# Optimization experiments

Hardware: AMD Instinct MI355X
Metric: run time of the kernel (lower is better)

## Reference

```python
import jax, jax.numpy as jnp
import numpy as np

B, T, C = 2, 2048, 1024
H, DH = 16, 64          # n_heads = d_model // 64
WIN = 256               # sliding window size
K = 32                  # n_oscillators
DFF = 4096              # d_ff_hidden
NEG = -1e9


def setup_inputs() -> dict:
    key = jax.random.key(0)
    ks = jax.random.split(key, 16)
    sC = 1.0 / np.sqrt(C)
    sF = 1.0 / np.sqrt(DFF)
    sK = 1.0 / np.sqrt(K)
    return {
        "x": jax.random.normal(ks[0], (B, T, C), jnp.float32),
        "norm1_w": jnp.ones((C,), jnp.float32),
        "qkv_w": jax.random.normal(ks[1], (3 * C, C), jnp.float32) * sC,
        "qkv_b": jnp.zeros((3 * C,), jnp.float32),
        "proj_w": jax.random.normal(ks[2], (C, C), jnp.float32) * sC,
        "proj_b": jnp.zeros((C,), jnp.float32),
        "gate_w": jax.random.normal(ks[3], (1, C), jnp.float32) * 0.01,
        "gate_b": jnp.zeros((1,), jnp.float32),
        "trn_win": jax.random.normal(ks[4], (K, C), jnp.float32) * sC,
        "trn_wout": jax.random.normal(ks[5], (C, K), jnp.float32) * sK,
        "trn_gate_w": jax.random.normal(ks[6], (K, C), jnp.float32) * sC,
        "trn_gate_b": jnp.zeros((K,), jnp.float32),
        "trn_a_logit": jax.random.normal(ks[7], (K,), jnp.float32),
        "trn_theta": jax.random.uniform(ks[8], (K,), jnp.float32, 0.0, np.pi),
        "trn_res_scale": jnp.asarray(0.1, jnp.float32),
        "norm2_w": jnp.ones((C,), jnp.float32),
        "ffn_gate_w": jax.random.normal(ks[9], (DFF, C), jnp.float32) * sC,
        "ffn_up_w": jax.random.normal(ks[10], (DFF, C), jnp.float32) * sC,
        "ffn_down_w": jax.random.normal(ks[11], (C, DFF), jnp.float32) * sF,
    }


def _rms(z, w, eps=1e-6):
    return z * jax.lax.rsqrt(jnp.mean(z * z, axis=-1, keepdims=True) + eps) * w


def reference(x, norm1_w, qkv_w, qkv_b, proj_w, proj_b, gate_w, gate_b,
              trn_win, trn_wout, trn_gate_w, trn_gate_b, trn_a_logit,
              trn_theta, trn_res_scale, norm2_w, ffn_gate_w, ffn_up_w,
              ffn_down_w):
    h = _rms(x, norm1_w)

    # ---- windowed causal attention (dense mask, as in the original) ----
    qkv = h @ qkv_w.T + qkv_b                       # [B,T,3C]
    q, k, v = jnp.split(qkv, 3, axis=-1)
    heads = lambda t: t.reshape(B, T, H, DH).transpose(0, 2, 1, 3)  # [B,H,T,DH]
    q, k, v = heads(q), heads(k), heads(v)
    row = jnp.arange(T)[:, None]
    col = jnp.arange(T)[None, :]
    mask = jnp.where((col <= row) & (col >= row - WIN + 1), 0.0, NEG).astype(x.dtype)
    scores = jnp.einsum('bhqd,bhkd->bhqk', q, k) / jnp.sqrt(jnp.asarray(DH, x.dtype))
    attn = jax.nn.softmax(scores + mask, axis=-1)
    ao = jnp.einsum('bhqk,bhkd->bhqd', attn, v).transpose(0, 2, 1, 3).reshape(B, T, C)
    ao = ao @ proj_w.T + proj_b

    # ---- temporal resonance branch: K damped rotating oscillators ----
    u = h @ trn_win.T                               # [B,T,K] drive
    a = jax.nn.sigmoid(trn_a_logit)                 # amplitude in (0,1) (amplitude_max=1)
    ct, st = jnp.cos(trn_theta), jnp.sin(trn_theta)

    def step(carry, ut):
        sr, si = carry
        nsr = a * (ct * sr - st * si) + ut
        nsi = a * (st * sr + ct * si)
        return (nsr, nsi), nsr

    init = (jnp.zeros((B, K), x.dtype), jnp.zeros((B, K), x.dtype))
    _, ys = jax.lax.scan(step, init, u.transpose(1, 0, 2))  # ys: [T,B,K]
    y = ys.transpose(1, 0, 2)                                # [B,T,K]
    tg = jax.nn.sigmoid(h @ trn_gate_w.T + trn_gate_b)
    trn_out = ((tg * y) @ trn_wout.T) * trn_res_scale        # [B,T,C]

    # ---- sigmoid gate mix + residual ----
    g = jax.nn.sigmoid(h @ gate_w.T + gate_b)       # [B,T,1]
    x = x + g * ao + (1.0 - g) * trn_out

    # ---- SwiGLU FFN ----
    h2 = _rms(x, norm2_w)
    ffn = (jax.nn.silu(h2 @ ffn_gate_w.T) * (h2 @ ffn_up_w.T)) @ ffn_down_w.T
    return x + ffn
```

## Files before the change

### kernel.cpp

```cpp
#include <hip/hip_runtime.h>


typedef unsigned short u16;
typedef unsigned short u16x8 __attribute__((ext_vector_type(8)));
typedef __bf16 bf16x8 __attribute__((ext_vector_type(8)));
typedef float f32x4 __attribute__((ext_vector_type(4)));

#define DI static __device__ __forceinline__

DI u16 f2b(float f){
  union { float f; unsigned u; } v; v.f = f;
  unsigned r = v.u + 0x7FFFu + ((v.u >> 16) & 1u);
  return (u16)(r >> 16);
}
DI float b2f(u16 b){
  union { unsigned u; float f; } v; v.u = ((unsigned)b) << 16; return v.f;
}
DI u16x8 ld8(const u16* p){ return *(const u16x8*)p; }

DI f32x4 MFMA16(u16x8 a, u16x8 b, f32x4 c){
  return __builtin_amdgcn_mfma_f32_16x16x32_bf16(
      __builtin_bit_cast(bf16x8, a), __builtin_bit_cast(bf16x8, b), c, 0, 0, 0);
}

DI void async16(const void* g, void* l){
  void* gg = const_cast<void*>(g);
  __builtin_amdgcn_global_load_lds(
      (__attribute__((address_space(1))) void*)gg,
      (__attribute__((address_space(3))) void*)l, 16, 0, 0);
}

__global__ __launch_bounds__(256) void convert_w(
    const float* __restrict__ qkvw, const float* __restrict__ projw,
    const float* __restrict__ fgw, const float* __restrict__ fuw,
    const float* __restrict__ fdw, const float* __restrict__ twin,
    const float* __restrict__ tgw, const float* __restrict__ twout,
    u16* __restrict__ dst)
{
  size_t i = (size_t)blockIdx.x * 256 + threadIdx.x;
  if (i >= 4260352u) return;
  size_t e = i * 4;
  float4 v;
  if (e < 3145728u)        v = *(const float4*)(qkvw + e);
  else if (e < 4194304u)   v = *(const float4*)(projw + (e - 3145728u));
  else if (e < 12582912u){
    size_t i2 = e - 4194304u;
    int row = (int)(i2 >> 10), c = (int)(i2 & 1023);
    int G = row >> 5, j = row & 31;
    const float* src = (j < 16) ? fgw : fuw;
    v = *(const float4*)(src + (size_t)(G * 16 + (j & 15)) * 1024 + c);
  }
  else if (e < 16777216u)  v = *(const float4*)(fdw + (e - 12582912u));
  else if (e < 16908288u){
    size_t i2 = e - 16777216u;
    int row = (int)(i2 >> 10), c = (int)(i2 & 1023);
    if (row < 32)      v = *(const float4*)(twin + row * 1024 + c);
    else if (row < 64) v = *(const float4*)(tgw + (row - 32) * 1024 + c);
    else               v = make_float4(0.f, 0.f, 0.f, 0.f);
  } else {
    v = *(const float4*)(twout + (e - 16908288u));
  }
  uint2 p;
  p.x = (unsigned)f2b(v.x) | ((unsigned)f2b(v.y) << 16);
  p.y = (unsigned)f2b(v.z) | ((unsigned)f2b(v.w) << 16);
  *(uint2*)(dst + e) = p;
}

__global__ __launch_bounds__(256) void zero_f32(float* __restrict__ p, int n4)
{
  int i = blockIdx.x * 256 + threadIdx.x;
  if (i < n4) ((float4*)p)[i] = make_float4(0.f, 0.f, 0.f, 0.f);
}

__global__ __launch_bounds__(256) void rmsnorm_gate(
    const float* __restrict__ x, const float* __restrict__ w,
    const float* __restrict__ gw, const float* __restrict__ gb,
    u16* __restrict__ h, float* __restrict__ g)
{
  const int row = blockIdx.x, tid = threadIdx.x;
  const int wave = tid >> 6, lane = tid & 63;
  __shared__ float sb[8];
  float4 xv = ((const float4*)(x + (size_t)row * 1024))[tid];
  float ss = xv.x*xv.x + xv.y*xv.y + xv.z*xv.z + xv.w*xv.w;
#pragma unroll
  for (int m = 32; m; m >>= 1) ss += __shfl_xor(ss, m);
  if (lane == 0) sb[wave] = ss;
  __syncthreads();
  float rstd = rsqrtf((sb[0]+sb[1]+sb[2]+sb[3]) * (1.f/1024.f) + 1e-6f);
  float4 wv = ((const float4*)w)[tid];
  float h0 = xv.x*rstd*wv.x, h1 = xv.y*rstd*wv.y;
  float h2v = xv.z*rstd*wv.z, h3 = xv.w*rstd*wv.w;
  uint2 pk;
  pk.x = (unsigned)f2b(h0) | ((unsigned)f2b(h1) << 16);
  pk.y = (unsigned)f2b(h2v) | ((unsigned)f2b(h3) << 16);
  ((uint2*)(h + (size_t)row * 1024))[tid] = pk;
  float4 gv = ((const float4*)gw)[tid];
  float gd = h0*gv.x + h1*gv.y + h2v*gv.z + h3*gv.w;
#pragma unroll
  for (int m = 32; m; m >>= 1) gd += __shfl_xor(gd, m);
  if (lane == 0) sb[4 + wave] = gd;
  __syncthreads();
  if (tid == 0) g[row] = 1.f / (1.f + __expf(-(sb[4]+sb[5]+sb[6]+sb[7] + gb[0])));
}

__global__ __launch_bounds__(256) void reduce_mix_norm(
    const float* __restrict__ part, const float* __restrict__ x,
    const u16* __restrict__ trn, const float* __restrict__ g,
    const float* __restrict__ pb, const float* __restrict__ n2w,
    float* __restrict__ xmid, u16* __restrict__ h2)
{
  const int row = blockIdx.x, tid = threadIdx.x;
  const int wave = tid >> 6, lane = tid & 63;
  __shared__ float sb[4];
  const size_t ro = (size_t)row * 1024;
  float4 p0 = ((const float4*)(part + ro))[tid];
  float4 p1 = ((const float4*)(part + 4194304 + ro))[tid];
  float4 bb = ((const float4*)pb)[tid];
  float4 xv = ((const float4*)(x + ro))[tid];
  uint2 tz = ((const uint2*)(trn + ro))[tid];
  float gg = g[row];
  float t0 = b2f((u16)tz.x), t1 = b2f((u16)(tz.x >> 16));
  float t2 = b2f((u16)tz.y), t3 = b2f((u16)(tz.y >> 16));
  float m0 = xv.x + gg*(p0.x+p1.x+bb.x) + (1.f-gg)*t0;
  float m1 = xv.y + gg*(p0.y+p1.y+bb.y) + (1.f-gg)*t1;
  float m2 = xv.z + gg*(p0.z+p1.z+bb.z) + (1.f-gg)*t2;
  float m3 = xv.w + gg*(p0.w+p1.w+bb.w) + (1.f-gg)*t3;
  float4 mo; mo.x = m0; mo.y = m1; mo.z = m2; mo.w = m3;
  ((float4*)(xmid + ro))[tid] = mo;
  float ss = m0*m0 + m1*m1 + m2*m2 + m3*m3;
#pragma unroll
  for (int m = 32; m; m >>= 1) ss += __shfl_xor(ss, m);
  if (lane == 0) sb[wave] = ss;
  __syncthreads();
  float rstd = rsqrtf((sb[0]+sb[1]+sb[2]+sb[3]) * (1.f/1024.f) + 1e-6f);
  float4 wv = ((const float4*)n2w)[tid];
  uint2 pk;
  pk.x = (unsigned)f2b(m0*rstd*wv.x) | ((unsigned)f2b(m1*rstd*wv.y) << 16);
  pk.y = (unsigned)f2b(m2*rstd*wv.z) | ((unsigned)f2b(m3*rstd*wv.w) << 16);
  ((uint2*)(h2 + ro))[tid] = pk;
}

__global__ __launch_bounds__(256) void reduce_down(
    const float* __restrict__ part, const float* __restrict__ xmid,
    float* __restrict__ out)
{
  size_t i = (size_t)blockIdx.x * 256 + threadIdx.x;
  float4 p0 = ((const float4*)part)[i];
  float4 p1 = ((const float4*)(part + 4194304))[i];
  float4 xv = ((const float4*)xmid)[i];
  float4 o;
  o.x = xv.x + p0.x + p1.x; o.y = xv.y + p0.y + p1.y;
  o.z = xv.z + p0.z + p1.z; o.w = xv.w + p0.w + p1.w;
  ((float4*)out)[i] = o;
}

template<int MODE>
__global__ __launch_bounds__(256) void gemm_bt(
    const u16* __restrict__ A, const u16* __restrict__ B,
    float* __restrict__ outF, float* __restrict__ outF2, u16* __restrict__ outB,
    const float* __restrict__ bias, const float* __restrict__ auxF,
    int M, int N, int K)
{
  __shared__ __align__(16) u16 sA[128 * 32];
  __shared__ __align__(16) u16 sB[128 * 32];
  const int tid = threadIdx.x;
  const int wave = tid >> 6, lane = tid & 63;
  const int lr = lane & 15, lq = lane >> 4;
  const int m0 = blockIdx.x * 128, n0 = blockIdx.y * 128;
  const int wm = (wave & 1) * 64, wn = (wave >> 1) * 64;
  const int ks = K / (int)gridDim.z;
  const int kbeg = (int)blockIdx.z * ks, kend = kbeg + ks;
  f32x4 acc[4][4] = {};
  const int srow = wave * 16 + (lane >> 2);
  const int scol = (lane & 3) * 8;
  const u16* gA = A + (size_t)(m0 + srow) * K + scol;
  const u16* gB = B + (size_t)(n0 + srow) * K + scol;
  u16* lA0 = &sA[(wave * 16) * 32];
  u16* lA1 = &sA[(64 + wave * 16) * 32];
  u16* lB0 = &sB[(wave * 16) * 32];
  u16* lB1 = &sB[(64 + wave * 16) * 32];
  const size_t K64 = (size_t)64 * K;

  for (int k0 = kbeg; k0 < kend; k0 += 32){
    async16(gA + k0,       lA0);
    async16(gA + K64 + k0, lA1);
    async16(gB + k0,       lB0);
    async16(gB + K64 + k0, lB1);
    __syncthreads();
    u16x8 af[4], bf[4];
#pragma unroll
    for (int i = 0; i < 4; i++) af[i] = ld8(&sA[(wm + i*16 + lr)*32 + lq*8]);
#pragma unroll
    for (int i = 0; i < 4; i++) bf[i] = ld8(&sB[(wn + i*16 + lr)*32 + lq*8]);
#pragma unroll
    for (int mi = 0; mi < 4; mi++)
#pragma unroll
      for (int ni = 0; ni < 4; ni++)
        acc[mi][ni] = MFMA16(af[mi], bf[ni], acc[mi][ni]);
    __syncthreads();
  }

  if (MODE == 7){
    const int cb = ((n0 + wn) >> 1) + lr;
#pragma unroll
    for (int mi = 0; mi < 4; mi++){
      const int row = m0 + wm + mi*16 + lq*4;
#pragma unroll
      for (int p = 0; p < 2; p++){
        const int col = cb + p*16;
#pragma unroll
        for (int r = 0; r < 4; r++){
          float gv = acc[mi][2*p][r], uv = acc[mi][2*p+1][r];
          float rv = gv / (1.f + __expf(-gv)) * uv;
          outB[(size_t)(row + r) * (N >> 1) + col] = f2b(rv);
        }
      }
    }
    return;
  }

  float scale6 = 0.f;
  if (MODE == 6) scale6 = auxF[0];

#pragma unroll
  for (int mi = 0; mi < 4; mi++){
    const int row = m0 + wm + mi*16 + lq*4;
#pragma unroll
    for (int ni = 0; ni < 4; ni++){
      const int col = n0 + wn + ni*16 + lr;
#pragma unroll
      for (int r = 0; r < 4; r++){
        const int rr = row + r;
        float v = acc[mi][ni][r];
        if (MODE == 0){
          outB[(size_t)rr * N + col] = f2b(v + bias[col]);
        } else if (MODE == 5){
          int bb = rr >> 11, tt = rr & 2047;
          if (col < 32) atomicAdd(&outF[((size_t)bb * 32 + col) * 2048 + tt], v);
          else if (col < 64) atomicAdd(&outF2[(size_t)rr * 32 + (col - 32)], v);
        } else if (MODE == 6){
          outB[(size_t)rr * N + col] = f2b(v * scale6);
        } else if (MODE == 8){
          outF[(size_t)blockIdx.z * (size_t)M + (size_t)rr * N + col] = v;
        }
      }
    }
  }
}

__global__ __launch_bounds__(256) void attn_win(
    const u16* __restrict__ qkv, u16* __restrict__ ao)
{
  const int blk = blockIdx.x;
  const int tile = blk & 31, hh = (blk >> 5) & 15, b = blk >> 9;
  const int t0 = tile * 64;
  const int tid = threadIdx.x, wave = tid >> 6, lane = tid & 63;
  const int lr = lane & 15, lq = lane >> 4;
  const int qt = t0 + wave * 16;
  __shared__ __align__(16) u16 sVt[64 * 40];
  __shared__ __align__(16) u16 sP[4][16 * 32];

  const u16* base = qkv + (size_t)b * 2048 * 3072 + hh * 64;
  const u16* qrow = base + (size_t)(qt + lr) * 3072 + lq * 8;
  u16x8 qf0 = ld8(qrow), qf1 = ld8(qrow + 32);
  const u16* kbase = base + 1024;
  const u16* vbase = base + 2048;

  f32x4 o0 = {0,0,0,0}, o1 = {0,0,0,0}, o2 = {0,0,0,0}, o3 = {0,0,0,0};
  float mrun[4] = {-1e30f, -1e30f, -1e30f, -1e30f};
  float lrun[4] = {0.f, 0.f, 0.f, 0.f};
  const float c1 = 0.125f * 1.44269504088896f;

  const int kb = (t0 >= 256) ? (t0 - 256) : 0;
  const int ntl = (t0 + 64 - kb) >> 5;
  for (int it = 0; it < ntl; ++it){
    const int kt = kb + it * 32;
    __syncthreads();
    if (tid < 128){
      const int key = tid & 31, dh = tid >> 5;
      const u16* gv = vbase + (size_t)(kt + key) * 3072 + dh * 16;
      u16x8 v0 = ld8(gv), v1 = ld8(gv + 8);
#pragma unroll
      for (int j = 0; j < 8; j++){
        sVt[(dh*16 + j)     * 40 + key] = v0[j];
        sVt[(dh*16 + 8 + j) * 40 + key] = v1[j];
      }
    }
    __syncthreads();
    const bool active = (kt < qt + 16) && (kt + 286 >= qt);
    if (!active) continue;

    f32x4 s0 = {0,0,0,0}, s1 = {0,0,0,0};
    {
      const u16* kr = kbase + (size_t)(kt + lr) * 3072 + lq * 8;
      u16x8 k00 = ld8(kr), k01 = ld8(kr + 32);
      const u16* kr1 = kr + (size_t)16 * 3072;
      u16x8 k10 = ld8(kr1), k11 = ld8(kr1 + 32);
      s0 = MFMA16(qf0, k00, s0); s0 = MFMA16(qf1, k01, s0);
      s1 = MFMA16(qf0, k10, s1); s1 = MFMA16(qf1, k11, s1);
    }
    float al[4];
#pragma unroll
    for (int r = 0; r < 4; r++){
      const int q = qt + lq * 4 + r;
      const int ca = kt + lr, cb = kt + 16 + lr;
      float a0 = (ca <= q && ca + 255 >= q) ? s0[r] : -1e30f;
      float a1 = (cb <= q && cb + 255 >= q) ? s1[r] : -1e30f;
      float mx = fmaxf(a0, a1);
      mx = fmaxf(mx, __shfl_xor(mx, 1));
      mx = fmaxf(mx, __shfl_xor(mx, 2));
      mx = fmaxf(mx, __shfl_xor(mx, 4));
      mx = fmaxf(mx, __shfl_xor(mx, 8));
      float mn = fmaxf(mrun[r], mx);
      al[r] = exp2f((mrun[r] - mn) * c1);
      mrun[r] = mn;
      float p0 = (a0 > -1e29f) ? exp2f((a0 - mn) * c1) : 0.f;
      float p1 = (a1 > -1e29f) ? exp2f((a1 - mn) * c1) : 0.f;
      float sm = p0 + p1;
      sm += __shfl_xor(sm, 1); sm += __shfl_xor(sm, 2);
      sm += __shfl_xor(sm, 4); sm += __shfl_xor(sm, 8);
      lrun[r] = lrun[r] * al[r] + sm;
      sP[wave][(lq*4 + r) * 32 + lr]      = f2b(p0);
      sP[wave][(lq*4 + r) * 32 + 16 + lr] = f2b(p1);
    }
#pragma unroll
    for (int r = 0; r < 4; r++){
      o0[r] *= al[r]; o1[r] *= al[r]; o2[r] *= al[r]; o3[r] *= al[r];
    }
    __builtin_amdgcn_s_waitcnt(0xc07f);
    u16x8 pf = ld8(&sP[wave][lr * 32 + lq * 8]);
    o0 = MFMA16(pf, ld8(&sVt[(lr)      * 40 + lq * 8]), o0);
    o1 = MFMA16(pf, ld8(&sVt[(16 + lr) * 40 + lq * 8]), o1);
    o2 = MFMA16(pf, ld8(&sVt[(32 + lr) * 40 + lq * 8]), o2);
    o3 = MFMA16(pf, ld8(&sVt[(48 + lr) * 40 + lq * 8]), o3);
  }

  u16* aor = ao + (size_t)(b * 2048 + qt + lq * 4) * 1024 + hh * 64 + lr;
#pragma unroll
  for (int r = 0; r < 4; r++){
    float inv = 1.f / lrun[r];
    u16* p = aor + (size_t)r * 1024;
    p[0]  = f2b(o0[r] * inv);
    p[16] = f2b(o1[r] * inv);
    p[32] = f2b(o2[r] * inv);
    p[48] = f2b(o3[r] * inv);
  }
}

__global__ __launch_bounds__(256) void scan_k(
    const float* __restrict__ u_t, const float* __restrict__ tgl,
    const float* __restrict__ tgb,
    const float* __restrict__ alog, const float* __restrict__ theta,
    u16* __restrict__ z)
{
  const int bk = blockIdx.x;
  const int b = bk >> 5, k = bk & 31;
  const int j = threadIdx.x;
  const float a = 1.f / (1.f + __expf(-alog[k]));
  const float th = theta[k];
  const float bk_bias = tgb[k];
  const float wr = a * __cosf(th), wi = a * __sinf(th);
  const float* ubp = u_t + ((size_t)b * 32 + k) * 2048 + j * 8;
  float4 ua = ((const float4*)ubp)[0];
  float4 ub4 = ((const float4*)ubp)[1];
  float ur[8] = {ua.x, ua.y, ua.z, ua.w, ub4.x, ub4.y, ub4.z, ub4.w};
  float sr = 0.f, si = 0.f;
#pragma unroll
  for (int i = 0; i < 8; i++){
    float nr = wr*sr - wi*si + ur[i];
    float ni = wi*sr + wr*si;
    sr = nr; si = ni;
  }
  float w2r = wr*wr - wi*wi, w2i = 2.f*wr*wi;
  float w4r = w2r*w2r - w2i*w2i, w4i = 2.f*w2r*w2i;
  float Ar = w4r*w4r - w4i*w4i, Ai = 2.f*w4r*w4i;
  __shared__ float4 sc[256];
  float4 cur; cur.x = Ar; cur.y = Ai; cur.z = sr; cur.w = si;
  sc[j] = cur;
  __syncthreads();
  for (int s = 1; s < 256; s <<= 1){
    float4 pv;
    const bool has = (j >= s);
    if (has) pv = sc[j - s];
    __syncthreads();
    if (has){
      float nar = cur.x*pv.x - cur.y*pv.y;
      float nai = cur.x*pv.y + cur.y*pv.x;
      float nbr = cur.x*pv.z - cur.y*pv.w + cur.z;
      float nbi = cur.x*pv.w + cur.y*pv.z + cur.w;
      cur.x = nar; cur.y = nai; cur.z = nbr; cur.w = nbi;
    }
    sc[j] = cur;
    __syncthreads();
  }
  float s_r = 0.f, s_i = 0.f;
  if (j > 0){ float4 pr = sc[j - 1]; s_r = pr.z; s_i = pr.w; }
  const float* tgp = tgl + ((size_t)b * 2048 + j * 8) * 32 + k;
  u16* zp = z + ((size_t)b * 2048 + j * 8) * 32 + k;
#pragma unroll
  for (int i = 0; i < 8; i++){
    float nr = wr*s_r - wi*s_i + ur[i];
    float ni = wi*s_r + wr*s_i;
    s_r = nr; s_i = ni;
    float tgv = 1.f / (1.f + __expf(-(tgp[(size_t)i * 32] + bk_bias)));
    zp[(size_t)i * 32] = f2b(s_r * tgv);
  }
}

extern "C" void kernel_launch(void* const* d_in, const int* in_sizes, int n_in,
                              void* d_out, int out_size, void* d_ws, size_t ws_size,
                              hipStream_t stream)
{
  (void)in_sizes; (void)n_in; (void)out_size; (void)ws_size;
  const float* x      = (const float*)d_in[0];
  const float* n1w    = (const float*)d_in[1];
  const float* qkvw   = (const float*)d_in[2];
  const float* qkvb   = (const float*)d_in[3];
  const float* projw  = (const float*)d_in[4];
  const float* projb  = (const float*)d_in[5];
  const float* gatew  = (const float*)d_in[6];
  const float* gateb  = (const float*)d_in[7];
  const float* twin   = (const float*)d_in[8];
  const float* twout  = (const float*)d_in[9];
  const float* tgw    = (const float*)d_in[10];
  const float* tgb    = (const float*)d_in[11];
  const float* talog  = (const float*)d_in[12];
  const float* ttheta = (const float*)d_in[13];
  const float* tscale = (const float*)d_in[14];
  const float* n2w    = (const float*)d_in[15];
  const float* fgw    = (const float*)d_in[16];
  const float* fuw    = (const float*)d_in[17];
  const float* fdw    = (const float*)d_in[18];
  float* out = (float*)d_out;

  char* wsb = (char*)d_ws;
  size_t off = 0;
  auto take = [&](size_t bytes) -> void* {
    void* r = wsb + off; off += (bytes + 255) & ~(size_t)255; return r;
  };
  u16*   wall = (u16*)take(17041408ull * 2);
  u16*   h    = (u16*)take(4194304ull * 2);
  u16*   h2   = (u16*)take(4194304ull * 2);
  u16*   trn  = (u16*)take(4194304ull * 2);
  float* g    = (float*)take(4096ull * 4);
  float* xmid = (float*)take(4194304ull * 4);
  float* uacc = (float*)take(262144ull * 4);
  float* tgl  = uacc + 131072;
  u16*   zz   = (u16*)take(131072ull * 2);
  u16*   regA = (u16*)take(4096ull * 4096 * 2);
  u16*   regB = (u16*)take(4096ull * 4096 * 2);

  u16* wq  = wall;
  u16* wp  = wall + 3145728;
  u16* wgu = wall + 4194304;
  u16* wd  = wall + 12582912;
  u16* wct = wall + 16777216;
  u16* wo  = wall + 16908288;
  u16*   qkv   = regA;
  float* pproj = (float*)regA;
  u16*   act   = regA;
  u16*   ao    = regB;
  float* pdown = (float*)regB;

  convert_w<<<16642, 256, 0, stream>>>(qkvw, projw, fgw, fuw, fdw, twin, tgw, twout, wall);
  rmsnorm_gate<<<4096, 256, 0, stream>>>(x, n1w, gatew, gateb, h, g);
  zero_f32<<<256, 256, 0, stream>>>(uacc, 65536);
  gemm_bt<5><<<dim3(32, 1, 8), 256, 0, stream>>>(h, wct, uacc, tgl, nullptr, nullptr,
                                                 nullptr, 0, 128, 1024);
  scan_k<<<64, 256, 0, stream>>>(uacc, tgl, tgb, talog, ttheta, zz);
  gemm_bt<6><<<dim3(32, 8), 256, 0, stream>>>(zz, wo, nullptr, nullptr, trn, nullptr,
                                              tscale, 0, 1024, 32);
  gemm_bt<0><<<dim3(32, 24), 256, 0, stream>>>(h, wq, nullptr, nullptr, qkv, qkvb,
                                               nullptr, 0, 3072, 1024);
  attn_win<<<1024, 256, 0, stream>>>(qkv, ao);
  gemm_bt<8><<<dim3(32, 8, 2), 256, 0, stream>>>(ao, wp, pproj, nullptr, nullptr, nullptr,
                                                 nullptr, 4194304, 1024, 1024);
  reduce_mix_norm<<<4096, 256, 0, stream>>>(pproj, x, trn, g, projb, n2w, xmid, h2);
  gemm_bt<7><<<dim3(32, 64), 256, 0, stream>>>(h2, wgu, nullptr, nullptr, act, nullptr,
                                               nullptr, 0, 8192, 1024);
  gemm_bt<8><<<dim3(32, 8, 2), 256, 0, stream>>>(act, wd, pdown, nullptr, nullptr, nullptr,
                                                 nullptr, 4194304, 1024, 4096);
  reduce_down<<<4096, 256, 0, stream>>>(pdown, xmid, out);
}
```

Before: 449.6 us.

## Fuse TRN projections into QKV GEMM, widen K-step, atomically accumulate FFN down

Folds the oscillator drive and gate projections into extra columns of the QKV GEMM, so the separate zero-fill and atomic projection GEMM disappear, and moves the gate sigmoid into that epilogue. GEMMs gain a WIDE mode that loads two 32-wide K slabs per barrier pair, halving synchronisation. The FFN down projection now atomically adds into the output, which already holds the residual, with a 4-way K split, removing the reduce_down kernel and the xmid buffer. The attention V-transpose load is also spread across all 256 threads. The atomics make the results order-nondeterministic and add contention.

```diff
diff --git a/kernel.cpp b/kernel.cpp
--- a/kernel.cpp
+++ b/kernel.cpp
@@ -38,38 +38,31 @@
     u16* __restrict__ dst)
 {
   size_t i = (size_t)blockIdx.x * 256 + threadIdx.x;
-  if (i >= 4260352u) return;
+  if (i >= 4235264u) return;
   size_t e = i * 4;
   float4 v;
   if (e < 3145728u)        v = *(const float4*)(qkvw + e);
-  else if (e < 4194304u)   v = *(const float4*)(projw + (e - 3145728u));
-  else if (e < 12582912u){
-    size_t i2 = e - 4194304u;
+  else if (e < 3276800u){
+    size_t i2 = e - 3145728u;
+    int row = (int)(i2 >> 10), c = (int)(i2 & 1023);
+    if (row < 32)      v = *(const float4*)(twin + row * 1024 + c);
+    else if (row < 64) v = *(const float4*)(tgw + (row - 32) * 1024 + c);
+    else               v = make_float4(0.f, 0.f, 0.f, 0.f);
+  }
+  else if (e < 4325376u)   v = *(const float4*)(projw + (e - 3276800u));
+  else if (e < 12713984u){
+    size_t i2 = e - 4325376u;
     int row = (int)(i2 >> 10), c = (int)(i2 & 1023);
     int G = row >> 5, j = row & 31;
     const float* src = (j < 16) ? fgw : fuw;
     v = *(const float4*)(src + (size_t)(G * 16 + (j & 15)) * 1024 + c);
   }
-  else if (e < 16777216u)  v = *(const float4*)(fdw + (e - 12582912u));
-  else if (e < 16908288u){
-    size_t i2 = e - 16777216u;
-    int row = (int)(i2 >> 10), c = (int)(i2 & 1023);
-    if (row < 32)      v = *(const float4*)(twin + row * 1024 + c);
-    else if (row < 64) v = *(const float4*)(tgw + (row - 32) * 1024 + c);
-    else               v = make_float4(0.f, 0.f, 0.f, 0.f);
-  } else {
-    v = *(const float4*)(twout + (e - 16908288u));
-  }
+  else if (e < 16908288u)  v = *(const float4*)(fdw + (e - 12713984u));
+  else                     v = *(const float4*)(twout + (e - 16908288u));
   uint2 p;
   p.x = (unsigned)f2b(v.x) | ((unsigned)f2b(v.y) << 16);
   p.y = (unsigned)f2b(v.z) | ((unsigned)f2b(v.w) << 16);
   *(uint2*)(dst + e) = p;
-}
-
-__global__ __launch_bounds__(256) void zero_f32(float* __restrict__ p, int n4)
-{
-  int i = blockIdx.x * 256 + threadIdx.x;
-  if (i < n4) ((float4*)p)[i] = make_float4(0.f, 0.f, 0.f, 0.f);
 }
 
 __global__ __launch_bounds__(256) void rmsnorm_gate(
@@ -107,7 +100,7 @@
     const float* __restrict__ part, const float* __restrict__ x,
     const u16* __restrict__ trn, const float* __restrict__ g,
     const float* __restrict__ pb, const float* __restrict__ n2w,
-    float* __restrict__ xmid, u16* __restrict__ h2)
+    float* __restrict__ out, u16* __restrict__ h2)
 {
   const int row = blockIdx.x, tid = threadIdx.x;
   const int wave = tid >> 6, lane = tid & 63;
@@ -126,7 +119,7 @@
   float m2 = xv.z + gg*(p0.z+p1.z+bb.z) + (1.f-gg)*t2;
   float m3 = xv.w + gg*(p0.w+p1.w+bb.w) + (1.f-gg)*t3;
   float4 mo; mo.x = m0; mo.y = m1; mo.z = m2; mo.w = m3;
-  ((float4*)(xmid + ro))[tid] = mo;
+  ((float4*)(out + ro))[tid] = mo;
   float ss = m0*m0 + m1*m1 + m2*m2 + m3*m3;
 #pragma unroll
   for (int m = 32; m; m >>= 1) ss += __shfl_xor(ss, m);
@@ -140,29 +133,15 @@
   ((uint2*)(h2 + ro))[tid] = pk;
 }
 
-__global__ __launch_bounds__(256) void reduce_down(
-    const float* __restrict__ part, const float* __restrict__ xmid,
-    float* __restrict__ out)
-{
-  size_t i = (size_t)blockIdx.x * 256 + threadIdx.x;
-  float4 p0 = ((const float4*)part)[i];
-  float4 p1 = ((const float4*)(part + 4194304))[i];
-  float4 xv = ((const float4*)xmid)[i];
-  float4 o;
-  o.x = xv.x + p0.x + p1.x; o.y = xv.y + p0.y + p1.y;
-  o.z = xv.z + p0.z + p1.z; o.w = xv.w + p0.w + p1.w;
-  ((float4*)out)[i] = o;
-}
-
-template<int MODE>
+template<int MODE, bool WIDE>
 __global__ __launch_bounds__(256) void gemm_bt(
     const u16* __restrict__ A, const u16* __restrict__ B,
     float* __restrict__ outF, float* __restrict__ outF2, u16* __restrict__ outB,
     const float* __restrict__ bias, const float* __restrict__ auxF,
     int M, int N, int K)
 {
-  __shared__ __align__(16) u16 sA[128 * 32];
-  __shared__ __align__(16) u16 sB[128 * 32];
+  __shared__ __align__(16) u16 sA[2][128 * 32];
+  __shared__ __align__(16) u16 sB[2][128 * 32];
   const int tid = threadIdx.x;
   const int wave = tid >> 6, lane = tid & 63;
   const int lr = lane & 15, lq = lane >> 4;
@@ -175,29 +154,64 @@
   const int scol = (lane & 3) * 8;
   const u16* gA = A + (size_t)(m0 + srow) * K + scol;
   const u16* gB = B + (size_t)(n0 + srow) * K + scol;
-  u16* lA0 = &sA[(wave * 16) * 32];
-  u16* lA1 = &sA[(64 + wave * 16) * 32];
-  u16* lB0 = &sB[(wave * 16) * 32];
-  u16* lB1 = &sB[(64 + wave * 16) * 32];
+  u16* lA0 = &sA[0][(wave * 16) * 32];
+  u16* lA1 = &sA[0][(64 + wave * 16) * 32];
+  u16* lB0 = &sB[0][(wave * 16) * 32];
+  u16* lB1 = &sB[0][(64 + wave * 16) * 32];
   const size_t K64 = (size_t)64 * K;
-
-  for (int k0 = kbeg; k0 < kend; k0 += 32){
-    async16(gA + k0,       lA0);
-    async16(gA + K64 + k0, lA1);
-    async16(gB + k0,       lB0);
-    async16(gB + K64 + k0, lB1);
-    __syncthreads();
-    u16x8 af[4], bf[4];
-#pragma unroll
-    for (int i = 0; i < 4; i++) af[i] = ld8(&sA[(wm + i*16 + lr)*32 + lq*8]);
-#pragma unroll
-    for (int i = 0; i < 4; i++) bf[i] = ld8(&sB[(wn + i*16 + lr)*32 + lq*8]);
-#pragma unroll
-    for (int mi = 0; mi < 4; mi++)
-#pragma unroll
-      for (int ni = 0; ni < 4; ni++)
-        acc[mi][ni] = MFMA16(af[mi], bf[ni], acc[mi][ni]);
-    __syncthreads();
+  const int BUF = 128 * 32;
+
+  if (WIDE){
+    for (int k0 = kbeg; k0 < kend; k0 += 64){
+      async16(gA + k0,            lA0);
+      async16(gA + K64 + k0,      lA1);
+      async16(gB + k0,            lB0);
+      async16(gB + K64 + k0,      lB1);
+      async16(gA + k0 + 32,       lA0 + BUF);
+      async16(gA + K64 + k0 + 32, lA1 + BUF);
+      async16(gB + k0 + 32,       lB0 + BUF);
+      async16(gB + K64 + k0 + 32, lB1 + BUF);
+      __syncthreads();
+      u16x8 af[4], bf[4];
+#pragma unroll
+      for (int i = 0; i < 4; i++) af[i] = ld8(&sA[0][(wm + i*16 + lr)*32 + lq*8]);
+#pragma unroll
+      for (int i = 0; i < 4; i++) bf[i] = ld8(&sB[0][(wn + i*16 + lr)*32 + lq*8]);
+#pragma unroll
+      for (int mi = 0; mi < 4; mi++)
+#pragma unroll
+        for (int ni = 0; ni < 4; ni++)
+          acc[mi][ni] = MFMA16(af[mi], bf[ni], acc[mi][ni]);
+#pragma unroll
+      for (int i = 0; i < 4; i++) af[i] = ld8(&sA[1][(wm + i*16 + lr)*32 + lq*8]);
+#pragma unroll
+      for (int i = 0; i < 4; i++) bf[i] = ld8(&sB[1][(wn + i*16 + lr)*32 + lq*8]);
+#pragma unroll
+      for (int mi = 0; mi < 4; mi++)
+#pragma unroll
+        for (int ni = 0; ni < 4; ni++)
+          acc[mi][ni] = MFMA16(af[mi], bf[ni], acc[mi][ni]);
+      __syncthreads();
+    }
+  } else {
+    for (int k0 = kbeg; k0 < kend; k0 += 32){
+      async16(gA + k0,       lA0);
+      async16(gA + K64 + k0, lA1);
+      async16(gB + k0,       lB0);
+      async16(gB + K64 + k0, lB1);
+      __syncthreads();
+      u16x8 af[4], bf[4];
+#pragma unroll
+      for (int i = 0; i < 4; i++) af[i] = ld8(&sA[0][(wm + i*16 + lr)*32 + lq*8]);
+#pragma unroll
+      for (int i = 0; i < 4; i++) bf[i] = ld8(&sB[0][(wn + i*16 + lr)*32 + lq*8]);
+#pragma unroll
+      for (int mi = 0; mi < 4; mi++)
+#pragma unroll
+        for (int ni = 0; ni < 4; ni++)
+          acc[mi][ni] = MFMA16(af[mi], bf[ni], acc[mi][ni]);
+      __syncthreads();
+    }
   }
 
   if (MODE == 7){
@@ -233,11 +247,18 @@
         const int rr = row + r;
         float v = acc[mi][ni][r];
         if (MODE == 0){
-          outB[(size_t)rr * N + col] = f2b(v + bias[col]);
-        } else if (MODE == 5){
-          int bb = rr >> 11, tt = rr & 2047;
-          if (col < 32) atomicAdd(&outF[((size_t)bb * 32 + col) * 2048 + tt], v);
-          else if (col < 64) atomicAdd(&outF2[(size_t)rr * 32 + (col - 32)], v);
+          if (n0 < 3072){
+            outB[(size_t)rr * 3072 + col] = f2b(v + bias[col]);
+          } else {
+            int c2 = col - 3072;
+            int bb = rr >> 11, tt = rr & 2047;
+            if (c2 < 32) outF[((size_t)bb * 32 + c2) * 2048 + tt] = v;
+            else if (c2 < 64)
+              outF2[(size_t)rr * 32 + (c2 - 32)] =
+                  1.f / (1.f + __expf(-(v + auxF[c2 - 32])));
+          }
+        } else if (MODE == 3){
+          atomicAdd(&outF[(size_t)rr * N + col], v);
         } else if (MODE == 6){
           outB[(size_t)rr * N + col] = f2b(v * scale6);
         } else if (MODE == 8){
@@ -276,15 +297,13 @@
   for (int it = 0; it < ntl; ++it){
     const int kt = kb + it * 32;
     __syncthreads();
-    if (tid < 128){
-      const int key = tid & 31, dh = tid >> 5;
-      const u16* gv = vbase + (size_t)(kt + key) * 3072 + dh * 16;
-      u16x8 v0 = ld8(gv), v1 = ld8(gv + 8);
-#pragma unroll
-      for (int j = 0; j < 8; j++){
-        sVt[(dh*16 + j)     * 40 + key] = v0[j];
-        sVt[(dh*16 + 8 + j) * 40 + key] = v1[j];
-      }
+    {
+      const int key = tid & 31, dseg = tid >> 5;
+      const u16* gv = vbase + (size_t)(kt + key) * 3072 + dseg * 8;
+      u16x8 v0 = ld8(gv);
+#pragma unroll
+      for (int j = 0; j < 8; j++)
+        sVt[(dseg*8 + j) * 40 + key] = v0[j];
     }
     __syncthreads();
     const bool active = (kt < qt + 16) && (kt + 286 >= qt);
@@ -348,8 +367,7 @@
 }
 
 __global__ __launch_bounds__(256) void scan_k(
-    const float* __restrict__ u_t, const float* __restrict__ tgl,
-    const float* __restrict__ tgb,
+    const float* __restrict__ u_t, const float* __restrict__ tg,
     const float* __restrict__ alog, const float* __restrict__ theta,
     u16* __restrict__ z)
 {
@@ -358,7 +376,6 @@
   const int j = threadIdx.x;
   const float a = 1.f / (1.f + __expf(-alog[k]));
   const float th = theta[k];
-  const float bk_bias = tgb[k];
   const float wr = a * __cosf(th), wi = a * __sinf(th);
   const float* ubp = u_t + ((size_t)b * 32 + k) * 2048 + j * 8;
   float4 ua = ((const float4*)ubp)[0];
@@ -395,15 +412,14 @@
   }
   float s_r = 0.f, s_i = 0.f;
   if (j > 0){ float4 pr = sc[j - 1]; s_r = pr.z; s_i = pr.w; }
-  const float* tgp = tgl + ((size_t)b * 2048 + j * 8) * 32 + k;
+  const float* tgp = tg + ((size_t)b * 2048 + j * 8) * 32 + k;
   u16* zp = z + ((size_t)b * 2048 + j * 8) * 32 + k;
 #pragma unroll
   for (int i = 0; i < 8; i++){
     float nr = wr*s_r - wi*s_i + ur[i];
     float ni = wi*s_r + wr*s_i;
     s_r = nr; s_i = ni;
-    float tgv = 1.f / (1.f + __expf(-(tgp[(size_t)i * 32] + bk_bias)));
-    zp[(size_t)i * 32] = f2b(s_r * tgv);
+    zp[(size_t)i * 32] = f2b(s_r * tgp[(size_t)i * 32]);
   }
 }
 
@@ -438,47 +454,40 @@
   auto take = [&](size_t bytes) -> void* {
     void* r = wsb + off; off += (bytes + 255) & ~(size_t)255; return r;
   };
-  u16*   wall = (u16*)take(17041408ull * 2);
+  u16*   wall = (u16*)take(16941056ull * 2);
   u16*   h    = (u16*)take(4194304ull * 2);
   u16*   h2   = (u16*)take(4194304ull * 2);
   u16*   trn  = (u16*)take(4194304ull * 2);
   float* g    = (float*)take(4096ull * 4);
-  float* xmid = (float*)take(4194304ull * 4);
-  float* uacc = (float*)take(262144ull * 4);
-  float* tgl  = uacc + 131072;
+  float* u_t  = (float*)take(131072ull * 4);
+  float* tg   = (float*)take(131072ull * 4);
   u16*   zz   = (u16*)take(131072ull * 2);
   u16*   regA = (u16*)take(4096ull * 4096 * 2);
   u16*   regB = (u16*)take(4096ull * 4096 * 2);
 
   u16* wq  = wall;
-  u16* wp  = wall + 3145728;
-  u16* wgu = wall + 4194304;
-  u16* wd  = wall + 12582912;
-  u16* wct = wall + 16777216;
+  u16* wp  = wall + 3276800;
+  u16* wgu = wall + 4325376;
+  u16* wd  = wall + 12713984;
   u16* wo  = wall + 16908288;
   u16*   qkv   = regA;
   float* pproj = (float*)regA;
-  u16*   act   = regA;
   u16*   ao    = regB;
-  float* pdown = (float*)regB;
-
-  convert_w<<<16642, 256, 0, stream>>>(qkvw, projw, fgw, fuw, fdw, twin, tgw, twout, wall);
+  u16*   act   = regB;
+
+  convert_w<<<16544, 256, 0, stream>>>(qkvw, projw, fgw, fuw, fdw, twin, tgw, twout, wall);
   rmsnorm_gate<<<4096, 256, 0, stream>>>(x, n1w, gatew, gateb, h, g);
-  zero_f32<<<256, 256, 0, stream>>>(uacc, 65536);
-  gemm_bt<5><<<dim3(32, 1, 8), 256, 0, stream>>>(h, wct, uacc, tgl, nullptr, nullptr,
-                                                 nullptr, 0, 128, 1024);
-  scan_k<<<64, 256, 0, stream>>>(uacc, tgl, tgb, talog, ttheta, zz);
-  gemm_bt<6><<<dim3(32, 8), 256, 0, stream>>>(zz, wo, nullptr, nullptr, trn, nullptr,
-                                              tscale, 0, 1024, 32);
-  gemm_bt<0><<<dim3(32, 24), 256, 0, stream>>>(h, wq, nullptr, nullptr, qkv, qkvb,
-                                               nullptr, 0, 3072, 1024);
+  gemm_bt<0, true><<<dim3(32, 25), 256, 0, stream>>>(h, wq, u_t, tg, qkv, qkvb,
+                                                     tgb, 0, 3200, 1024);
   attn_win<<<1024, 256, 0, stream>>>(qkv, ao);
-  gemm_bt<8><<<dim3(32, 8, 2), 256, 0, stream>>>(ao, wp, pproj, nullptr, nullptr, nullptr,
-                                                 nullptr, 4194304, 1024, 1024);
-  reduce_mix_norm<<<4096, 256, 0, stream>>>(pproj, x, trn, g, projb, n2w, xmid, h2);
-  gemm_bt<7><<<dim3(32, 64), 256, 0, stream>>>(h2, wgu, nullptr, nullptr, act, nullptr,
-                                               nullptr, 0, 8192, 1024);
-  gemm_bt<8><<<dim3(32, 8, 2), 256, 0, stream>>>(act, wd, pdown, nullptr, nullptr, nullptr,
-                                                 nullptr, 4194304, 1024, 4096);
-  reduce_down<<<4096, 256, 0, stream>>>(pdown, xmid, out);
-}
+  scan_k<<<64, 256, 0, stream>>>(u_t, tg, talog, ttheta, zz);
+  gemm_bt<6, false><<<dim3(32, 8), 256, 0, stream>>>(zz, wo, nullptr, nullptr, trn, nullptr,
+                                                     tscale, 0, 1024, 32);
+  gemm_bt<8, true><<<dim3(32, 8, 2), 256, 0, stream>>>(ao, wp, pproj, nullptr, nullptr, nullptr,
+                                                       nullptr, 4194304, 1024, 1024);
+  reduce_mix_norm<<<4096, 256, 0, stream>>>(pproj, x, trn, g, projb, n2w, out, h2);
+  gemm_bt<7, true><<<dim3(32, 64), 256, 0, stream>>>(h2, wgu, nullptr, nullptr, act, nullptr,
+                                                     nullptr, 0, 8192, 1024);
+  gemm_bt<3, true><<<dim3(32, 8, 4), 256, 0, stream>>>(act, wd, out, nullptr, nullptr, nullptr,
+                                                       nullptr, 0, 1024, 4096);
+}
```

Result: slower. 474.0 us (+5.4%).
